# Optimization experiments

Measured on AMD Instinct MI355X. Metric: run time of the kernel, lower is better.

Reference implementation:

```python
import jax, jax.numpy as jnp
import numpy as np

LAMBDA_K_TAU = 0.1
RIDGE = 0.1


def _masked_cov(x, mask, counts):
    """Covariance of masked rows. x: [B,S,D], mask: [B,S] float, counts: [B] float.
    Equivalent to packing the masked rows (batch_2d_tensor) then _torch_cov."""
    xm = x * mask[..., None]
    mean = xm.sum(axis=1) / counts[:, None]                 # [B,D]
    xc = (xm - mean[:, None, :]) * mask[..., None]          # [B,S,D]
    cov = jnp.einsum('bsi,bsj->bij', xc, xc)
    return cov / (counts - 1.0)[:, None, None]


def _calc_label_cov_inv(task_cov, label_cov):
    d = task_cov.shape[-1]
    eye = jnp.eye(d, dtype=task_cov.dtype)
    return jnp.linalg.inv(LAMBDA_K_TAU * label_cov + (1.0 - LAMBDA_K_TAU) * task_cov + RIDGE * eye)


def setup_inputs() -> dict:
    key = jax.random.key(0)
    ks = jax.random.split(key, 6)
    B, S, Q, D = 256, 512, 256, 512
    support_set = jax.random.normal(ks[0], (B, S, D), dtype=jnp.float32)
    support_labels = jax.random.randint(ks[1], (B, S), 0, 2, dtype=jnp.int32)
    query_set = jax.random.normal(ks[2], (B, Q, D), dtype=jnp.float32)
    # lengths in [len//2, len] so both classes are present and counts > 1
    support_set_lengths = jax.random.randint(ks[3], (B,), S // 2, S + 1, dtype=jnp.int32)
    query_set_lengths = jax.random.randint(ks[4], (B,), Q // 2, Q + 1, dtype=jnp.int32)
    log_prediction_scaling = jnp.asarray(np.log(10.0), dtype=jnp.float32)
    return {
        'support_set': support_set,
        'support_labels': support_labels,
        'query_set': query_set,
        'support_set_lengths': support_set_lengths,
        'query_set_lengths': query_set_lengths,
        'log_prediction_scaling': log_prediction_scaling,
    }


def reference(support_set, support_labels, query_set, support_set_lengths,
              query_set_lengths, log_prediction_scaling):
    B, S, D = support_set.shape
    Q = query_set.shape[1]
    f32 = support_set.dtype

    sup_valid = (jnp.arange(S)[None, :] < support_set_lengths[:, None]).astype(f32)  # [B,S]
    mask_pos = (support_labels == 1).astype(f32) * sup_valid                          # [B,S]
    mask_neg = (support_labels == 0).astype(f32) * sup_valid

    pos_counts = mask_pos.sum(axis=1)   # [B]
    neg_counts = mask_neg.sum(axis=1)
    sup_counts = support_set_lengths.astype(f32)

    positive_mean = jnp.einsum('bsd,bs->bd', support_set, mask_pos) / pos_counts[:, None]
    negative_mean = jnp.einsum('bsd,bs->bd', support_set, mask_neg) / neg_counts[:, None]

    cov_mats = _masked_cov(support_set, sup_valid, sup_counts)   # task covariance
    pos_mats = _masked_cov(support_set, mask_pos, pos_counts)    # == cov of packed positives
    neg_mats = _masked_cov(support_set, mask_neg, neg_counts)

    pos_inv = _calc_label_cov_inv(cov_mats, pos_mats)  # [B,D,D]
    neg_inv = _calc_label_cov_inv(cov_mats, neg_mats)

    q_valid = (jnp.arange(Q)[None, :] < query_set_lengths[:, None]).astype(f32)  # [B,Q]

    pos_diff = positive_mean[:, None, :] - query_set  # [B,Q,D]
    neg_diff = negative_mean[:, None, :] - query_set
    pos_maha = jnp.einsum('bik,bkx,bix->bi', pos_diff, pos_inv, pos_diff) * q_valid
    neg_maha = jnp.einsum('bik,bkx,bix->bi', neg_diff, neg_inv, neg_diff) * q_valid

    logit_scale = jnp.exp(log_prediction_scaling)
    # scale is applied inside batch_calculate_mahalanobis_logits AND again in forward
    logits = jnp.stack([neg_maha, pos_maha], axis=-1) * (-1.0) * logit_scale
    return logits * logit_scale  # [B,Q,2]
```

## Files before the change

kernel.cpp:

```cpp
#include <hip/hip_runtime.h>
#include <hip/hip_bf16.h>

#define TPB 256
constexpr int B_ = 256, S_ = 512, D_ = 512, Q_ = 256, NM_ = 512;
constexpr int NB = 64, NT = 8;

typedef _Float16 f16x8 __attribute__((ext_vector_type(8)));
typedef float f32x4 __attribute__((ext_vector_type(4)));

__device__ __forceinline__ int pidx(int j, int a){ return j*(15-j)/2 + (a-j-1); }

__device__ __forceinline__ void decode_mt(int bid, int W, int& m, int& t){
  int x = bid & 7, r = bid >> 3;
  t = r % W; int u = r / W;
  m = (((u >> 1)*8 + x) << 1) | (u & 1);
}

__device__ __forceinline__ void stage_D(const float* __restrict__ src, size_t ld,
                                        float (*dst)[68], int t)
{
  int r = t >> 2, seg = (t & 3) * 16;
  const float4* s4 = (const float4*)(src + (size_t)r*ld + seg);
  #pragma unroll
  for (int i=0;i<4;i++) *((float4*)&dst[r][seg + i*4]) = s4[i];
}

__device__ __forceinline__ void mm_acc68(const float (*Aop)[68], const float (*Bop)[68],
                                         float acc[4][4], int tr, int tc)
{
  for (int kk=0;kk<64;kk++){
    float4 av = *((const float4*)&Aop[kk][tr*4]);
    float4 bv = *((const float4*)&Bop[kk][tc*4]);
    float a[4]={av.x,av.y,av.z,av.w}, b2[4]={bv.x,bv.y,bv.z,bv.w};
    #pragma unroll
    for (int u=0;u<4;u++)
      #pragma unroll
      for (int v=0;v<4;v++) acc[u][v] = fmaf(a[u], b2[v], acc[u][v]);
  }
}

__global__ __launch_bounds__(1024) void k_stats(const float* __restrict__ X,
                                                const int* __restrict__ labels,
                                                const int* __restrict__ slen,
                                                float* __restrict__ mu,
                                                float* __restrict__ cnt,
                                                unsigned int* __restrict__ wpbits)
{
  int b = blockIdx.x, t = threadIdx.x;
  int td = t & 255, sg = t >> 8;
  __shared__ int lab[S_];
  __shared__ float red[1024];
  __shared__ float part[4][256][4];
  int L = slen[b];
  if (t < S_) {
    int lb = labels[b*S_ + t];
    lab[t] = (t < L) ? lb : -1;
  }
  __syncthreads();
  if (t < 16) {
    unsigned int wword = 0;
    for (int i2 = 0; i2 < 32; i2++) if (lab[t*32 + i2] == 1) wword |= (1u << i2);
    wpbits[b*16 + t] = wword;
  }
  red[t] = (t < S_) ? ((lab[t]==1) ? 1.f : 0.f) : 0.f;
  __syncthreads();
  for (int o=512;o>0;o>>=1){ if(t<o) red[t]+=red[t+o]; __syncthreads(); }
  float cp = red[0]; __syncthreads();
  red[t] = (t < S_) ? ((lab[t]==0) ? 1.f : 0.f) : 0.f;
  __syncthreads();
  for (int o=512;o>0;o>>=1){ if(t<o) red[t]+=red[t+o]; __syncthreads(); }
  float cn = red[0];
  if (t==0){ cnt[b*2+0]=cn; cnt[b*2+1]=cp; }
  float sp0=0,sp1=0,sn0=0,sn1=0;
  const float* Xb = X + (size_t)b*S_*D_;
  for (int s=sg*128; s<sg*128+128; s++){
    int e = lab[s];
    if (e < 0) continue;
    float x0 = Xb[(size_t)s*D_ + td];
    float x1 = Xb[(size_t)s*D_ + td + 256];
    if (e==1){ sp0+=x0; sp1+=x1; } else { sn0+=x0; sn1+=x1; }
  }
  part[sg][td][0]=sn0; part[sg][td][1]=sn1; part[sg][td][2]=sp0; part[sg][td][3]=sp1;
  __syncthreads();
  if (sg == 0){
    float a0=0,a1=0,a2=0,a3=0;
    #pragma unroll
    for (int g=0;g<4;g++){ a0+=part[g][td][0]; a1+=part[g][td][1]; a2+=part[g][td][2]; a3+=part[g][td][3]; }
    float stv = (float)L;
    float* mb = mu + (size_t)b*3*D_;
    mb[0*D_ + td] = a0/cn;      mb[0*D_ + td+256] = a1/cn;
    mb[1*D_ + td] = a2/cp;      mb[1*D_ + td+256] = a3/cp;
    mb[2*D_ + td] = (a0+a2)/stv; mb[2*D_ + td+256] = (a1+a3)/stv;
  }
}

__global__ __launch_bounds__(TPB) void k_prep(const float* __restrict__ X,
                                              const int* __restrict__ slen,
                                              unsigned short* __restrict__ Xvh,
                                              unsigned short* __restrict__ Xvl)
{
  int b = blockIdx.y, z = blockIdx.x;
  int d0 = (z>>3)*64, s0 = (z&7)*64;
  int t = threadIdx.x;
  __shared__ float Tl[64][65];
  const float* src = X + ((size_t)b*S_ + s0)*D_ + d0;
  { int r = t>>2, seg = (t&3)*16;
    const float4* s4 = (const float4*)(src + (size_t)r*D_ + seg);
    #pragma unroll
    for (int i=0;i<4;i++){ float4 v = s4[i];
      Tl[seg+i*4+0][r]=v.x; Tl[seg+i*4+1][r]=v.y; Tl[seg+i*4+2][r]=v.z; Tl[seg+i*4+3][r]=v.w; } }
  __syncthreads();
  int L = slen[b];
  int dr = t>>2, sc = (t&3)*16;
  union U16 { unsigned short u[8]; uint4 v; };
  U16 H[2], Lo[2];
  #pragma unroll
  for (int g=0; g<2; g++)
    #pragma unroll
    for (int i=0;i<8;i++){
      int si = sc + g*8 + i;
      float x = (s0+si < L) ? Tl[dr][si] : 0.f;
      _Float16 hh = (_Float16)x;
      float lo = x - (float)hh;
      H[g].u[i]  = __builtin_bit_cast(unsigned short, hh);
      Lo[g].u[i] = __builtin_bit_cast(unsigned short, (_Float16)lo);
    }
  size_t o = ((size_t)b*D_ + d0+dr)*S_ + s0 + sc;
  *(uint4*)(Xvh+o)   = H[0].v;  *(uint4*)(Xvh+o+8) = H[1].v;
  *(uint4*)(Xvl+o)   = Lo[0].v; *(uint4*)(Xvl+o+8) = Lo[1].v;
}

__global__ __launch_bounds__(TPB,2) void k_gram(const unsigned short* __restrict__ Xvh,
                                                const unsigned short* __restrict__ Xvl,
                                                const unsigned int* __restrict__ wpbits,
                                                const float* __restrict__ mu,
                                                const float* __restrict__ cnt,
                                                const int* __restrict__ slen,
                                                float* __restrict__ A)
{
  __shared__ unsigned short sAvh[128][32], sAvl[128][32], sAph[128][32], sApl[128][32],
                            sBvh[128][32], sBvl[128][32];
  int id = blockIdx.x;
  int g = id>>3;
  int b = (g/10)*8 + (id&7);
  int z = g%10;
  int ti=0; while (z >= 4-ti){ z -= 4-ti; ti++; } int tj = ti + z;
  int i0 = ti*128, j0 = tj*128;
  int t = threadIdx.x, lane = t&63, w = t>>6;
  int wr = w>>1, wc = w&1, l15 = lane&15;

  f32x4 acc_t[4][4], acc_p[4][4];
  f32x4 z4 = {0.f,0.f,0.f,0.f};
  #pragma unroll
  for (int mf=0;mf<4;mf++)
    #pragma unroll
    for (int nf=0;nf<4;nf++){ acc_t[mf][nf]=z4; acc_p[mf][nf]=z4; }

  const size_t baseA = ((size_t)b*D_ + i0)*S_;
  const size_t baseB = ((size_t)b*D_ + j0)*S_;
  int phx = (lane>>4) ^ ((l15>>1)&3);

  for (int ks=0; ks<16; ks++){
    int s0 = ks*32;
    unsigned int wpw = wpbits[b*16 + ks];
    __syncthreads();
    #pragma unroll
    for (int h=0; h<2; h++){
      int ci = t + h*256;
      int row = ci>>2, cpos = ci&3;
      int ph = cpos ^ ((row>>1)&3);
      size_t ga = baseA + (size_t)row*S_ + s0 + cpos*8;
      size_t gb = baseB + (size_t)row*S_ + s0 + cpos*8;
      uint4 vh = *(const uint4*)(Xvh+ga);
      uint4 vl = *(const uint4*)(Xvl+ga);
      uint4 bh = *(const uint4*)(Xvh+gb);
      uint4 bl = *(const uint4*)(Xvl+gb);
      unsigned int m8 = (wpw >> (cpos*8)) & 0xFFu;
      uint4 mk;
      mk.x = ((m8&1u)?0xFFFFu:0u)  | ((m8&2u)?0xFFFF0000u:0u);
      mk.y = ((m8&4u)?0xFFFFu:0u)  | ((m8&8u)?0xFFFF0000u:0u);
      mk.z = ((m8&16u)?0xFFFFu:0u) | ((m8&32u)?0xFFFF0000u:0u);
      mk.w = ((m8&64u)?0xFFFFu:0u) | ((m8&128u)?0xFFFF0000u:0u);
      uint4 p4, q4;
      p4.x = vh.x&mk.x; p4.y = vh.y&mk.y; p4.z = vh.z&mk.z; p4.w = vh.w&mk.w;
      q4.x = vl.x&mk.x; q4.y = vl.y&mk.y; q4.z = vl.z&mk.z; q4.w = vl.w&mk.w;
      *(uint4*)&sAvh[row][ph*8] = vh;
      *(uint4*)&sAvl[row][ph*8] = vl;
      *(uint4*)&sAph[row][ph*8] = p4;
      *(uint4*)&sApl[row][ph*8] = q4;
      *(uint4*)&sBvh[row][ph*8] = bh;
      *(uint4*)&sBvl[row][ph*8] = bl;
    }
    __syncthreads();
    f16x8 Avh[4], Avl[4], Aph[4], Apl[4];
    #pragma unroll
    for (int mf=0;mf<4;mf++){
      int r = wr*64 + mf*16 + l15;
      Avh[mf] = __builtin_bit_cast(f16x8, *(const uint4*)&sAvh[r][phx*8]);
      Avl[mf] = __builtin_bit_cast(f16x8, *(const uint4*)&sAvl[r][phx*8]);
      Aph[mf] = __builtin_bit_cast(f16x8, *(const uint4*)&sAph[r][phx*8]);
      Apl[mf] = __builtin_bit_cast(f16x8, *(const uint4*)&sApl[r][phx*8]);
    }
    #pragma unroll
    for (int nf=0;nf<4;nf++){
      int r = wc*64 + nf*16 + l15;
      f16x8 Bh = __builtin_bit_cast(f16x8, *(const uint4*)&sBvh[r][phx*8]);
      f16x8 Bl = __builtin_bit_cast(f16x8, *(const uint4*)&sBvl[r][phx*8]);
      #pragma unroll
      for (int mf=0;mf<4;mf++){
        acc_t[mf][nf] = __builtin_amdgcn_mfma_f32_16x16x32_f16(Avh[mf], Bh, acc_t[mf][nf],0,0,0);
        acc_t[mf][nf] = __builtin_amdgcn_mfma_f32_16x16x32_f16(Avh[mf], Bl, acc_t[mf][nf],0,0,0);
        acc_t[mf][nf] = __builtin_amdgcn_mfma_f32_16x16x32_f16(Avl[mf], Bh, acc_t[mf][nf],0,0,0);
        acc_p[mf][nf] = __builtin_amdgcn_mfma_f32_16x16x32_f16(Aph[mf], Bh, acc_p[mf][nf],0,0,0);
        acc_p[mf][nf] = __builtin_amdgcn_mfma_f32_16x16x32_f16(Aph[mf], Bl, acc_p[mf][nf],0,0,0);
        acc_p[mf][nf] = __builtin_amdgcn_mfma_f32_16x16x32_f16(Apl[mf], Bh, acc_p[mf][nf],0,0,0);
      }
    }
  }
  float cn = cnt[b*2+0], cp = cnt[b*2+1];
  float stv = (float)slen[b];
  float kn = 0.1f/(cn-1.f), kp = 0.1f/(cp-1.f), kt = 0.9f/(stv-1.f);
  float rn = 0.1f*cn/(cn-1.f), rp = 0.1f*cp/(cp-1.f), rt = 0.9f*stv/(stv-1.f);
  const float* mb = mu + (size_t)b*3*D_;
  float* A0 = A + (size_t)(b*2+0)*D_*D_;
  float* A1 = A + (size_t)(b*2+1)*D_*D_;
  int rbase = i0 + wr*64 + (lane>>4)*4;
  int cbase = j0 + wc*64 + l15;
  #pragma unroll
  for (int mf=0;mf<4;mf++){
    #pragma unroll
    for (int i=0;i<4;i++){
      int r = rbase + mf*16 + i;
      float mnr = mb[r], mpr = mb[D_+r], mtr = mb[2*D_+r];
      #pragma unroll
      for (int nf=0;nf<4;nf++){
        int c = cbase + nf*16;
        float mnc = mb[c], mpc = mb[D_+c], mtc = mb[2*D_+c];
        float gp = acc_p[mf][nf][i];
        float gt = acc_t[mf][nf][i];
        float gn = gt - gp;
        float diag = (r==c)?0.1f:0.f;
        A0[(size_t)r*D_ + c] = kn*gn + kt*gt - rn*mnr*mnc - rt*mtr*mtc + diag;
        A1[(size_t)r*D_ + c] = kp*gp + kt*gt - rp*mpr*mpc - rt*mtr*mtc + diag;
      }
    }
  }
}

__global__ __launch_bounds__(TPB) void k_diag(float* __restrict__ A,
                                              float* __restrict__ invDT, int j)
{
  int m, t0; decode_mt(blockIdx.x, 1, m, t0); (void)t0;
  int t = threadIdx.x;
  __shared__ float Ld[64][65];
  __shared__ float Iv[64][65];
  float* Ab = A + (size_t)m*D_*D_ + (size_t)(j*NB)*D_ + j*NB;
  for (int l=t; l<4096; l+=TPB){ int r=l>>6, c=l&63; Ld[r][c] = Ab[(size_t)r*D_ + c]; Iv[r][c] = 0.f; }
  __syncthreads();
  for (int k=0;k<64;k++){
    if (t==0) Ld[k][k] = sqrtf(Ld[k][k]);
    __syncthreads();
    if (t>k && t<64) Ld[t][k] /= Ld[k][k];
    __syncthreads();
    for (int l=t; l<4096; l+=TPB){
      int r=l>>6, c=l&63;
      if (r>k && c>k) Ld[r][c] = fmaf(-Ld[r][k], Ld[c][k], Ld[r][c]);
    }
    __syncthreads();
  }
  if (t < 64){
    int c = t;
    Iv[c][c] = 1.f/Ld[c][c];
    for (int r=c+1;r<64;r++){
      float s = 0.f;
      for (int k2=c;k2<r;k2++) s += Ld[r][k2]*Iv[k2][c];
      Iv[r][c] = -s/Ld[r][r];
    }
  }
  __syncthreads();
  float* Ib = invDT + ((size_t)m*8 + j)*4096;
  for (int l=t; l<4096; l+=TPB){ Ib[l] = Iv[l&63][l>>6]; }
}

__global__ __launch_bounds__(TPB) void k_panel(float* __restrict__ A,
                                               const float* __restrict__ invDT,
                                               unsigned short* __restrict__ Ut,
                                               int j, int W)
{
  int m, ti; decode_mt(blockIdx.x, W, m, ti);
  int ib = j + 1 + ti;
  int t = threadIdx.x, tr = t&15, tc = t>>4;
  __shared__ float Ta[64][68], Tb[64][68];
  float* U = A + (size_t)m*D_*D_ + (size_t)(j*NB)*D_ + ib*NB;
  stage_D(invDT + ((size_t)m*8 + j)*4096, 64, Ta, t);
  stage_D(U, D_, Tb, t);
  __syncthreads();
  float acc[4][4] = {};
  mm_acc68(Ta, Tb, acc, tr, tc);
  #pragma unroll
  for (int u=0;u<4;u++){
    float4 o = make_float4(acc[u][0],acc[u][1],acc[u][2],acc[u][3]);
    *((float4*)(U + (size_t)(tr*4+u)*D_ + tc*4)) = o;
  }
  __syncthreads();
  unsigned short* shh = (unsigned short*)Ta;
  unsigned short* shl = (unsigned short*)Tb;
  #pragma unroll
  for (int u=0;u<4;u++)
    #pragma unroll
    for (int v=0;v<4;v++){
      float val = acc[u][v];
      _Float16 h = (_Float16)val;
      float lo = val - (float)h;
      shh[(tc*4+v)*72 + tr*4+u] = __builtin_bit_cast(unsigned short, h);
      shl[(tc*4+v)*72 + tr*4+u] = __builtin_bit_cast(unsigned short, (_Float16)lo);
    }
  __syncthreads();
  unsigned short* Ub = Ut + ((size_t)m*28 + pidx(j, ib)) * 8192;
  { int r = t>>2, cs = (t&3)*16;
    *(uint4*)(Ub + r*64 + cs)          = *(uint4*)&shh[r*72 + cs];
    *(uint4*)(Ub + r*64 + cs + 8)      = *(uint4*)&shh[r*72 + cs + 8];
    *(uint4*)(Ub + 4096 + r*64 + cs)   = *(uint4*)&shl[r*72 + cs];
    *(uint4*)(Ub + 4096 + r*64 + cs+8) = *(uint4*)&shl[r*72 + cs + 8];
  }
}

__device__ __forceinline__ void trail_stage(const unsigned short* __restrict__ Ua,
                                            const unsigned short* __restrict__ Ub,
                                            unsigned short (*Ah)[72], unsigned short (*Al)[72],
                                            unsigned short (*Bh)[72], unsigned short (*Bl)[72],
                                            int t)
{
  int r = t>>2, cs = (t&3)*16;
  *(uint4*)&Ah[r][cs]   = *(const uint4*)(Ua + r*64 + cs);
  *(uint4*)&Ah[r][cs+8] = *(const uint4*)(Ua + r*64 + cs + 8);
  *(uint4*)&Al[r][cs]   = *(const uint4*)(Ua + 4096 + r*64 + cs);
  *(uint4*)&Al[r][cs+8] = *(const uint4*)(Ua + 4096 + r*64 + cs + 8);
  *(uint4*)&Bh[r][cs]   = *(const uint4*)(Ub + r*64 + cs);
  *(uint4*)&Bh[r][cs+8] = *(const uint4*)(Ub + r*64 + cs + 8);
  *(uint4*)&Bl[r][cs]   = *(const uint4*)(Ub + 4096 + r*64 + cs);
  *(uint4*)&Bl[r][cs+8] = *(const uint4*)(Ub + 4096 + r*64 + cs + 8);
}

__device__ __forceinline__ void trail_mfma(const unsigned short (*Ah)[72], const unsigned short (*Al)[72],
                                           const unsigned short (*Bh)[72], const unsigned short (*Bl)[72],
                                           f32x4 acc[4], int w, int l15, int lk)
{
  #pragma unroll
  for (int s=0;s<2;s++){
    f16x8 Afh = __builtin_bit_cast(f16x8, *(const uint4*)&Ah[w*16 + l15][s*32 + lk*8]);
    f16x8 Afl = __builtin_bit_cast(f16x8, *(const uint4*)&Al[w*16 + l15][s*32 + lk*8]);
    #pragma unroll
    for (int ni=0;ni<4;ni++){
      f16x8 Bfh = __builtin_bit_cast(f16x8, *(const uint4*)&Bh[ni*16 + l15][s*32 + lk*8]);
      f16x8 Bfl = __builtin_bit_cast(f16x8, *(const uint4*)&Bl[ni*16 + l15][s*32 + lk*8]);
      acc[ni] = __builtin_amdgcn_mfma_f32_16x16x32_f16(Afh, Bfh, acc[ni],0,0,0);
      acc[ni] = __builtin_amdgcn_mfma_f32_16x16x32_f16(Afh, Bfl, acc[ni],0,0,0);
      acc[ni] = __builtin_amdgcn_mfma_f32_16x16x32_f16(Afl, Bfh, acc[ni],0,0,0);
    }
  }
}

__device__ __forceinline__ void trail_rmw(float* __restrict__ Cb, const f32x4 acc[4],
                                          int w, int l15, int lk)
{
  #pragma unroll
  for (int ni=0;ni<4;ni++)
    #pragma unroll
    for (int i=0;i<4;i++){
      int r = w*16 + lk*4 + i, cc = ni*16 + l15;
      float* pC = Cb + (size_t)r*D_ + cc;
      *pC -= acc[ni][i];
    }
}

__global__ __launch_bounds__(TPB) void k_trailrow(float* __restrict__ A,
                                                  const unsigned short* __restrict__ Ut,
                                                  int j, int row, int W)
{
  int m, z; decode_mt(blockIdx.x, W, m, z);
  int b2 = row + z;
  int t = threadIdx.x, lane = t&63, w = t>>6, l15 = lane&15, lk = lane>>4;
  __shared__ unsigned short Ah[64][72], Al[64][72], Bh[64][72], Bl[64][72];
  const unsigned short* Um = Ut + (size_t)m*28*8192;
  trail_stage(Um + (size_t)pidx(j,row)*8192, Um + (size_t)pidx(j,b2)*8192, Ah, Al, Bh, Bl, t);
  __syncthreads();
  f32x4 acc[4];
  #pragma unroll
  for (int ni=0;ni<4;ni++) acc[ni] = (f32x4){0.f,0.f,0.f,0.f};
  trail_mfma(Ah, Al, Bh, Bl, acc, w, l15, lk);
  float* Cb = A + (size_t)m*D_*D_ + (size_t)(row*NB)*D_ + b2*NB;
  trail_rmw(Cb, acc, w, l15, lk);
}

__global__ __launch_bounds__(TPB) void k_trail2(float* __restrict__ A,
                                                const unsigned short* __restrict__ Ut,
                                                int jb, int W)
{
  int m, z; decode_mt(blockIdx.x, W, m, z);
  int base = jb + 2;
  int Tn = NT - base;
  int p = 0, zz = z;
  while (zz >= Tn - p){ zz -= Tn - p; p++; }
  int a2 = base + p, b2 = a2 + zz;
  int t = threadIdx.x, lane = t&63, w = t>>6, l15 = lane&15, lk = lane>>4;
  __shared__ unsigned short Ah[64][72], Al[64][72], Bh[64][72], Bl[64][72];
  const unsigned short* Um = Ut + (size_t)m*28*8192;
  f32x4 acc[4];
  #pragma unroll
  for (int ni=0;ni<4;ni++) acc[ni] = (f32x4){0.f,0.f,0.f,0.f};
  #pragma unroll
  for (int c=0;c<2;c++){
    int j = jb + c;
    __syncthreads();
    trail_stage(Um + (size_t)pidx(j,a2)*8192, Um + (size_t)pidx(j,b2)*8192, Ah, Al, Bh, Bl, t);
    __syncthreads();
    trail_mfma(Ah, Al, Bh, Bl, acc, w, l15, lk);
  }
  float* Cb = A + (size_t)m*D_*D_ + (size_t)(a2*NB)*D_ + b2*NB;
  trail_rmw(Cb, acc, w, l15, lk);
}

__global__ __launch_bounds__(TPB) void k_solvefin(const float* __restrict__ Qs,
                                                  const float* __restrict__ mu,
                                                  const float* __restrict__ A,
                                                  const float* __restrict__ invDT,
                                                  float* __restrict__ Z,
                                                  const int* __restrict__ qlen,
                                                  const float* __restrict__ lps,
                                                  float* __restrict__ out)
{
  int m, t0; decode_mt(blockIdx.x, 4, m, t0);
  int q0 = t0*NB;
  int b = m>>1, cls = m&1;
  int t = threadIdx.x, tr = t&15, tc = t>>4;
  __shared__ float Ta[64][68], Tb[64][68];
  const float* Am = A + (size_t)m*D_*D_;
  float* Zm = Z + (size_t)m*D_*Q_;
  const float* muv = mu + ((size_t)b*3 + cls)*D_;
  float cs[4] = {0.f,0.f,0.f,0.f};
  for (int j=0;j<NT;j++){
    float acc[4][4];
    {
      float4 mv = *(const float4*)&muv[j*NB + tr*4];
      #pragma unroll
      for (int v=0;v<4;v++){
        float4 qv = *(const float4*)&Qs[((size_t)b*Q_ + q0 + tc*4 + v)*D_ + j*NB + tr*4];
        acc[0][v] = mv.x - qv.x;
        acc[1][v] = mv.y - qv.y;
        acc[2][v] = mv.z - qv.z;
        acc[3][v] = mv.w - qv.w;
      }
    }
    for (int k=0;k<j;k++){
      stage_D(Am + (size_t)(k*NB)*D_ + j*NB, D_, Ta, t);
      { int r = t >> 2, seg = (t & 3)*16;
        const float4* s4 = (const float4*)(Zm + (size_t)(k*NB + r)*Q_ + q0 + seg);
        #pragma unroll
        for (int i=0;i<4;i++) *((float4*)&Tb[r][seg + i*4]) = s4[i];
      }
      __syncthreads();
      for (int kk=0;kk<64;kk++){
        float4 av = *((const float4*)&Ta[kk][tr*4]);
        float4 bv = *((const float4*)&Tb[kk][tc*4]);
        float a[4]={av.x,av.y,av.z,av.w}, bb2[4]={bv.x,bv.y,bv.z,bv.w};
        #pragma unroll
        for (int u=0;u<4;u++)
          #pragma unroll
          for (int v=0;v<4;v++) acc[u][v] = fmaf(-a[u], bb2[v], acc[u][v]);
      }
      __syncthreads();
    }
    #pragma unroll
    for (int u=0;u<4;u++)
      #pragma unroll
      for (int v=0;v<4;v++) Tb[tr*4+u][tc*4+v] = acc[u][v];
    stage_D(invDT + ((size_t)m*8 + j)*4096, 64, Ta, t);
    __syncthreads();
    float o4[4][4] = {};
    for (int kk=0;kk<64;kk++){
      float4 av = *((const float4*)&Ta[kk][tr*4]);
      float4 bv = *((const float4*)&Tb[kk][tc*4]);
      float a[4]={av.x,av.y,av.z,av.w}, bb2[4]={bv.x,bv.y,bv.z,bv.w};
      #pragma unroll
      for (int u=0;u<4;u++)
        #pragma unroll
        for (int v=0;v<4;v++) o4[u][v] = fmaf(a[u], bb2[v], o4[u][v]);
    }
    if (j < NT-1){
      #pragma unroll
      for (int u=0;u<4;u++){
        float4 o = make_float4(o4[u][0], o4[u][1], o4[u][2], o4[u][3]);
        *((float4*)(Zm + (size_t)(j*NB + tr*4+u)*Q_ + q0 + tc*4)) = o;
      }
    }
    #pragma unroll
    for (int u=0;u<4;u++)
      #pragma unroll
      for (int v=0;v<4;v++) cs[v] = fmaf(o4[u][v], o4[u][v], cs[v]);
    __syncthreads();
  }
  float* red = &Ta[0][0];
  #pragma unroll
  for (int v=0;v<4;v++) red[(tc*4+v)*16 + tr] = cs[v];
  __syncthreads();
  if (t < 64){
    float s = 0.f;
    #pragma unroll
    for (int i=0;i<16;i++) s += red[t*16 + i];
    int q = q0 + t;
    float valid = (q < qlen[b]) ? 1.f : 0.f;
    float s2 = expf(2.f*lps[0]);
    out[((size_t)b*Q_ + q)*2 + cls] = -s2*s*valid;
  }
}

extern "C" void kernel_launch(void* const* d_in, const int* in_sizes, int n_in,
                              void* d_out, int out_size, void* d_ws, size_t ws_size,
                              hipStream_t stream) {
  (void)in_sizes; (void)n_in; (void)out_size;
  const float* X   = (const float*)d_in[0];
  const int*   lab = (const int*)d_in[1];
  const float* Qs  = (const float*)d_in[2];
  const int*   sl  = (const int*)d_in[3];
  const int*   ql  = (const int*)d_in[4];
  const float* lps = (const float*)d_in[5];
  float* out = (float*)d_out;

  float* A  = (float*)d_ws;
  float* Z  = A + (size_t)NM_*D_*D_;
  unsigned short* Xvh = (unsigned short*)Z;
  unsigned short* Xvl = Xvh + (size_t)B_*D_*S_;
  unsigned short* Ut  = (unsigned short*)Z;
  float* invDT = Z + (size_t)NM_*D_*Q_;
  float* mu   = invDT + (size_t)NM_*8*64*64;
  float* cnt  = mu + (size_t)B_*3*D_;
  unsigned int* wpbits = (unsigned int*)(cnt + B_*2);
  size_t need = (size_t)((char*)(wpbits + B_*16) - (char*)d_ws);
  if (ws_size < need) return;

  k_stats<<<dim3(B_), dim3(1024), 0, stream>>>(X, lab, sl, mu, cnt, wpbits);
  k_prep<<<dim3(64, B_), dim3(TPB), 0, stream>>>(X, sl, Xvh, Xvl);
  k_gram<<<dim3(2560), dim3(TPB), 0, stream>>>(Xvh, Xvl, wpbits, mu, cnt, sl, A);

  for (int j=0; j<NT; j+=2){
    k_diag<<<dim3(NM_), dim3(TPB), 0, stream>>>(A, invDT, j);
    int nb0 = NT-1-j;
    if (nb0 > 0){
      k_panel<<<dim3(NM_*nb0), dim3(TPB), 0, stream>>>(A, invDT, Ut, j, nb0);
      int wr = NT - (j+1);
      k_trailrow<<<dim3(NM_*wr), dim3(TPB), 0, stream>>>(A, Ut, j, j+1, wr);
      k_diag<<<dim3(NM_), dim3(TPB), 0, stream>>>(A, invDT, j+1);
      int nb1 = NT-1-(j+1);
      if (nb1 > 0){
        k_panel<<<dim3(NM_*nb1), dim3(TPB), 0, stream>>>(A, invDT, Ut, j+1, nb1);
        int Tn = NT - (j+2);
        int np = Tn*(Tn+1)/2;
        if (np > 0) k_trail2<<<dim3(NM_*np), dim3(TPB), 0, stream>>>(A, Ut, j, np);
      }
    }
  }

  k_solvefin<<<dim3(NM_*4), dim3(TPB), 0, stream>>>(Qs, mu, A, invDT, Z, ql, lps, out);
}
```

Before: 2.445 ms.

## Fuse diagonal Cholesky factor into trailing-update kernels and widen solve tiles

Removes the standalone diagonal-factor launches by having the trailing-update block that owns the next diagonal tile (z==0) apply its update in shared memory and factor/invert it in place, so that tile is never written back and re-read. The triangular inverse is parallelised across four lanes per column with shuffle reductions instead of one thread per column. The final solve kernel now handles 128 queries per block instead of 64, reusing each staged factor tile across twice as many columns. The trade-off is that the z==0 blocks become much longer than their siblings, the grid-stride structure creates tail imbalance, and the solve kernel uses more registers, which may lower occupancy.

New measurement: 2.681 ms. 1.1x slower.

```diff
diff --git a/kernel.cpp b/kernel.cpp
--- a/kernel.cpp
+++ b/kernel.cpp
@@ -247,39 +247,57 @@
   }
 }
 
-__global__ __launch_bounds__(TPB) void k_diag(float* __restrict__ A,
-                                              float* __restrict__ invDT, int j)
-{
-  int m, t0; decode_mt(blockIdx.x, 1, m, t0); (void)t0;
-  int t = threadIdx.x;
-  __shared__ float Ld[64][65];
-  __shared__ float Iv[64][65];
-  float* Ab = A + (size_t)m*D_*D_ + (size_t)(j*NB)*D_ + j*NB;
-  for (int l=t; l<4096; l+=TPB){ int r=l>>6, c=l&63; Ld[r][c] = Ab[(size_t)r*D_ + c]; Iv[r][c] = 0.f; }
-  __syncthreads();
+__device__ __forceinline__ void diag_finish(float* Ld, float* __restrict__ Ig, int t)
+{
   for (int k=0;k<64;k++){
-    if (t==0) Ld[k][k] = sqrtf(Ld[k][k]);
-    __syncthreads();
-    if (t>k && t<64) Ld[t][k] /= Ld[k][k];
+    if (t==0) Ld[k*68+k] = sqrtf(Ld[k*68+k]);
+    __syncthreads();
+    if (t>k && t<64) Ld[t*68+k] /= Ld[k*68+k];
     __syncthreads();
     for (int l=t; l<4096; l+=TPB){
       int r=l>>6, c=l&63;
-      if (r>k && c>k) Ld[r][c] = fmaf(-Ld[r][k], Ld[c][k], Ld[r][c]);
-    }
-    __syncthreads();
-  }
-  if (t < 64){
-    int c = t;
-    Iv[c][c] = 1.f/Ld[c][c];
-    for (int r=c+1;r<64;r++){
-      float s = 0.f;
-      for (int k2=c;k2<r;k2++) s += Ld[r][k2]*Iv[k2][c];
-      Iv[r][c] = -s/Ld[r][r];
-    }
-  }
-  __syncthreads();
-  float* Ib = invDT + ((size_t)m*8 + j)*4096;
-  for (int l=t; l<4096; l+=TPB){ Ib[l] = Iv[l&63][l>>6]; }
+      if (r>k && c>k) Ld[r*68+c] = fmaf(-Ld[r*68+k], Ld[c*68+k], Ld[r*68+c]);
+    }
+    __syncthreads();
+  }
+  int c = t>>2, s = t&3;
+  float myv[16];
+  #pragma unroll
+  for (int i=0;i<16;i++) myv[i] = 0.f;
+  if (s==0) myv[0] = 1.f/Ld[c*68+c];
+  for (int r=c+1;r<64;r++){
+    float partial = 0.f;
+    #pragma unroll
+    for (int idx=0; idx<16; idx++){
+      int k2 = c + s + 4*idx;
+      if (k2 < r) partial = fmaf(Ld[r*68+k2], myv[idx], partial);
+    }
+    partial += __shfl_xor(partial, 1, 64);
+    partial += __shfl_xor(partial, 2, 64);
+    float val = -partial / Ld[r*68+r];
+    int d = r - c;
+    #pragma unroll
+    for (int idx=0; idx<16; idx++)
+      if ((d & 3) == s && (d >> 2) == idx) myv[idx] = val;
+  }
+  #pragma unroll
+  for (int idx=0; idx<16; idx++){
+    int k2 = c + s + 4*idx;
+    if (k2 < 64) Ig[c*64 + k2] = myv[idx];
+  }
+}
+
+__global__ __launch_bounds__(TPB) void k_diag0(float* __restrict__ A, float* __restrict__ invDT)
+{
+  int m, du; decode_mt(blockIdx.x, 1, m, du); (void)du;
+  int t = threadIdx.x;
+  __shared__ float Ld[64*68];
+  const float* Cd = A + (size_t)m*D_*D_;
+  { int r = t>>2, seg = (t&3)*16;
+    #pragma unroll
+    for (int i=0;i<4;i++) *((float4*)&Ld[r*68 + seg + i*4]) = *((const float4*)(Cd + (size_t)r*D_ + seg + i*4)); }
+  __syncthreads();
+  diag_finish(Ld, invDT + (size_t)m*8*4096, t);
 }
 
 __global__ __launch_bounds__(TPB) void k_panel(float* __restrict__ A,
@@ -374,14 +392,37 @@
     }
 }
 
+__device__ __forceinline__ void fused_diag(float* __restrict__ A, float* __restrict__ invDT,
+                                           float* Ld, const f32x4 acc[4],
+                                           int m, int dblk, int t, int w, int l15, int lk)
+{
+  const float* Cd = A + (size_t)m*D_*D_ + (size_t)(dblk*NB)*D_ + dblk*NB;
+  { int r = t>>2, seg = (t&3)*16;
+    #pragma unroll
+    for (int i=0;i<4;i++) *((float4*)&Ld[r*68 + seg + i*4]) = *((const float4*)(Cd + (size_t)r*D_ + seg + i*4)); }
+  __syncthreads();
+  #pragma unroll
+  for (int ni=0;ni<4;ni++)
+    #pragma unroll
+    for (int i=0;i<4;i++)
+      Ld[(w*16 + lk*4 + i)*68 + ni*16 + l15] -= acc[ni][i];
+  __syncthreads();
+  diag_finish(Ld, invDT + ((size_t)m*8 + dblk)*4096, t);
+}
+
 __global__ __launch_bounds__(TPB) void k_trailrow(float* __restrict__ A,
                                                   const unsigned short* __restrict__ Ut,
+                                                  float* __restrict__ invDT,
                                                   int j, int row, int W)
 {
   int m, z; decode_mt(blockIdx.x, W, m, z);
   int b2 = row + z;
   int t = threadIdx.x, lane = t&63, w = t>>6, l15 = lane&15, lk = lane>>4;
-  __shared__ unsigned short Ah[64][72], Al[64][72], Bh[64][72], Bl[64][72];
+  __shared__ unsigned short sbuf[4*64*72];
+  unsigned short (*Ah)[72] = (unsigned short(*)[72])sbuf;
+  unsigned short (*Al)[72] = (unsigned short(*)[72])(sbuf + 64*72);
+  unsigned short (*Bh)[72] = (unsigned short(*)[72])(sbuf + 2*64*72);
+  unsigned short (*Bl)[72] = (unsigned short(*)[72])(sbuf + 3*64*72);
   const unsigned short* Um = Ut + (size_t)m*28*8192;
   trail_stage(Um + (size_t)pidx(j,row)*8192, Um + (size_t)pidx(j,b2)*8192, Ah, Al, Bh, Bl, t);
   __syncthreads();
@@ -389,12 +430,18 @@
   #pragma unroll
   for (int ni=0;ni<4;ni++) acc[ni] = (f32x4){0.f,0.f,0.f,0.f};
   trail_mfma(Ah, Al, Bh, Bl, acc, w, l15, lk);
-  float* Cb = A + (size_t)m*D_*D_ + (size_t)(row*NB)*D_ + b2*NB;
-  trail_rmw(Cb, acc, w, l15, lk);
+  if (z == 0){
+    __syncthreads();
+    fused_diag(A, invDT, (float*)sbuf, acc, m, row, t, w, l15, lk);
+  } else {
+    float* Cb = A + (size_t)m*D_*D_ + (size_t)(row*NB)*D_ + b2*NB;
+    trail_rmw(Cb, acc, w, l15, lk);
+  }
 }
 
 __global__ __launch_bounds__(TPB) void k_trail2(float* __restrict__ A,
                                                 const unsigned short* __restrict__ Ut,
+                                                float* __restrict__ invDT,
                                                 int jb, int W)
 {
   int m, z; decode_mt(blockIdx.x, W, m, z);
@@ -404,7 +451,11 @@
   while (zz >= Tn - p){ zz -= Tn - p; p++; }
   int a2 = base + p, b2 = a2 + zz;
   int t = threadIdx.x, lane = t&63, w = t>>6, l15 = lane&15, lk = lane>>4;
-  __shared__ unsigned short Ah[64][72], Al[64][72], Bh[64][72], Bl[64][72];
+  __shared__ unsigned short sbuf[4*64*72];
+  unsigned short (*Ah)[72] = (unsigned short(*)[72])sbuf;
+  unsigned short (*Al)[72] = (unsigned short(*)[72])(sbuf + 64*72);
+  unsigned short (*Bh)[72] = (unsigned short(*)[72])(sbuf + 2*64*72);
+  unsigned short (*Bl)[72] = (unsigned short(*)[72])(sbuf + 3*64*72);
   const unsigned short* Um = Ut + (size_t)m*28*8192;
   f32x4 acc[4];
   #pragma unroll
@@ -417,8 +468,13 @@
     __syncthreads();
     trail_mfma(Ah, Al, Bh, Bl, acc, w, l15, lk);
   }
-  float* Cb = A + (size_t)m*D_*D_ + (size_t)(a2*NB)*D_ + b2*NB;
-  trail_rmw(Cb, acc, w, l15, lk);
+  if (z == 0){
+    __syncthreads();
+    fused_diag(A, invDT, (float*)sbuf, acc, m, base, t, w, l15, lk);
+  } else {
+    float* Cb = A + (size_t)m*D_*D_ + (size_t)(a2*NB)*D_ + b2*NB;
+    trail_rmw(Cb, acc, w, l15, lk);
+  }
 }
 
 __global__ __launch_bounds__(TPB) void k_solvefin(const float* __restrict__ Qs,
@@ -430,81 +486,105 @@
                                                   const float* __restrict__ lps,
                                                   float* __restrict__ out)
 {
-  int m, t0; decode_mt(blockIdx.x, 4, m, t0);
-  int q0 = t0*NB;
+  int m, t0; decode_mt(blockIdx.x, 2, m, t0);
+  int q0 = t0*128;
   int b = m>>1, cls = m&1;
   int t = threadIdx.x, tr = t&15, tc = t>>4;
-  __shared__ float Ta[64][68], Tb[64][68];
+  __shared__ float Ta[64][68];
+  __shared__ float Tb[64][136];
   const float* Am = A + (size_t)m*D_*D_;
   float* Zm = Z + (size_t)m*D_*Q_;
   const float* muv = mu + ((size_t)b*3 + cls)*D_;
-  float cs[4] = {0.f,0.f,0.f,0.f};
+  float cs[2][4] = {};
   for (int j=0;j<NT;j++){
-    float acc[4][4];
+    float acc[2][4][4];
     {
       float4 mv = *(const float4*)&muv[j*NB + tr*4];
       #pragma unroll
-      for (int v=0;v<4;v++){
-        float4 qv = *(const float4*)&Qs[((size_t)b*Q_ + q0 + tc*4 + v)*D_ + j*NB + tr*4];
-        acc[0][v] = mv.x - qv.x;
-        acc[1][v] = mv.y - qv.y;
-        acc[2][v] = mv.z - qv.z;
-        acc[3][v] = mv.w - qv.w;
-      }
+      for (int h=0;h<2;h++)
+        #pragma unroll
+        for (int v=0;v<4;v++){
+          float4 qv = *(const float4*)&Qs[((size_t)b*Q_ + q0 + h*64 + tc*4 + v)*D_ + j*NB + tr*4];
+          acc[h][0][v] = mv.x - qv.x;
+          acc[h][1][v] = mv.y - qv.y;
+          acc[h][2][v] = mv.z - qv.z;
+          acc[h][3][v] = mv.w - qv.w;
+        }
     }
     for (int k=0;k<j;k++){
       stage_D(Am + (size_t)(k*NB)*D_ + j*NB, D_, Ta, t);
       { int r = t >> 2, seg = (t & 3)*16;
-        const float4* s4 = (const float4*)(Zm + (size_t)(k*NB + r)*Q_ + q0 + seg);
         #pragma unroll
-        for (int i=0;i<4;i++) *((float4*)&Tb[r][seg + i*4]) = s4[i];
+        for (int h=0;h<2;h++){
+          const float4* s4 = (const float4*)(Zm + (size_t)(k*NB + r)*Q_ + q0 + h*64 + seg);
+          #pragma unroll
+          for (int i=0;i<4;i++) *((float4*)&Tb[r][h*68 + seg + i*4]) = s4[i];
+        }
       }
       __syncthreads();
       for (int kk=0;kk<64;kk++){
         float4 av = *((const float4*)&Ta[kk][tr*4]);
-        float4 bv = *((const float4*)&Tb[kk][tc*4]);
-        float a[4]={av.x,av.y,av.z,av.w}, bb2[4]={bv.x,bv.y,bv.z,bv.w};
+        float4 bv0 = *((const float4*)&Tb[kk][tc*4]);
+        float4 bv1 = *((const float4*)&Tb[kk][68 + tc*4]);
+        float a[4]={av.x,av.y,av.z,av.w};
+        float b0[4]={bv0.x,bv0.y,bv0.z,bv0.w}, b1[4]={bv1.x,bv1.y,bv1.z,bv1.w};
         #pragma unroll
         for (int u=0;u<4;u++)
           #pragma unroll
-          for (int v=0;v<4;v++) acc[u][v] = fmaf(-a[u], bb2[v], acc[u][v]);
+          for (int v=0;v<4;v++){
+            acc[0][u][v] = fmaf(-a[u], b0[v], acc[0][u][v]);
+            acc[1][u][v] = fmaf(-a[u], b1[v], acc[1][u][v]);
+          }
       }
       __syncthreads();
     }
     #pragma unroll
-    for (int u=0;u<4;u++)
-      #pragma unroll
-      for (int v=0;v<4;v++) Tb[tr*4+u][tc*4+v] = acc[u][v];
+    for (int h=0;h<2;h++)
+      #pragma unroll
+      for (int u=0;u<4;u++)
+        #pragma unroll
+        for (int v=0;v<4;v++) Tb[tr*4+u][h*68 + tc*4+v] = acc[h][u][v];
     stage_D(invDT + ((size_t)m*8 + j)*4096, 64, Ta, t);
     __syncthreads();
-    float o4[4][4] = {};
+    float o4[2][4][4] = {};
     for (int kk=0;kk<64;kk++){
       float4 av = *((const float4*)&Ta[kk][tr*4]);
-      float4 bv = *((const float4*)&Tb[kk][tc*4]);
-      float a[4]={av.x,av.y,av.z,av.w}, bb2[4]={bv.x,bv.y,bv.z,bv.w};
+      float4 bv0 = *((const float4*)&Tb[kk][tc*4]);
+      float4 bv1 = *((const float4*)&Tb[kk][68 + tc*4]);
+      float a[4]={av.x,av.y,av.z,av.w};
+      float b0[4]={bv0.x,bv0.y,bv0.z,bv0.w}, b1[4]={bv1.x,bv1.y,bv1.z,bv1.w};
       #pragma unroll
       for (int u=0;u<4;u++)
         #pragma unroll
-        for (int v=0;v<4;v++) o4[u][v] = fmaf(a[u], bb2[v], o4[u][v]);
+        for (int v=0;v<4;v++){
+          o4[0][u][v] = fmaf(a[u], b0[v], o4[0][u][v]);
+          o4[1][u][v] = fmaf(a[u], b1[v], o4[1][u][v]);
+        }
     }
     if (j < NT-1){
       #pragma unroll
-      for (int u=0;u<4;u++){
-        float4 o = make_float4(o4[u][0], o4[u][1], o4[u][2], o4[u][3]);
-        *((float4*)(Zm + (size_t)(j*NB + tr*4+u)*Q_ + q0 + tc*4)) = o;
-      }
-    }
-    #pragma unroll
-    for (int u=0;u<4;u++)
-      #pragma unroll
-      for (int v=0;v<4;v++) cs[v] = fmaf(o4[u][v], o4[u][v], cs[v]);
-    __syncthreads();
-  }
-  float* red = &Ta[0][0];
-  #pragma unroll
-  for (int v=0;v<4;v++) red[(tc*4+v)*16 + tr] = cs[v];
-  __syncthreads();
-  if (t < 64){
+      for (int h=0;h<2;h++)
+        #pragma unroll
+        for (int u=0;u<4;u++){
+          float4 o = make_float4(o4[h][u][0], o4[h][u][1], o4[h][u][2], o4[h][u][3]);
+          *((float4*)(Zm + (size_t)(j*NB + tr*4+u)*Q_ + q0 + h*64 + tc*4)) = o;
+        }
+    }
+    #pragma unroll
+    for (int h=0;h<2;h++)
+      #pragma unroll
+      for (int u=0;u<4;u++)
+        #pragma unroll
+        for (int v=0;v<4;v++) cs[h][v] = fmaf(o4[h][u][v], o4[h][u][v], cs[h][v]);
+    __syncthreads();
+  }
+  float* red = &Tb[0][0];
+  #pragma unroll
+  for (int h=0;h<2;h++)
+    #pragma unroll
+    for (int v=0;v<4;v++) red[(h*64 + tc*4+v)*16 + tr] = cs[h][v];
+  __syncthreads();
+  if (t < 128){
     float s = 0.f;
     #pragma unroll
     for (int i=0;i<16;i++) s += red[t*16 + i];
@@ -543,23 +623,20 @@
   k_prep<<<dim3(64, B_), dim3(TPB), 0, stream>>>(X, sl, Xvh, Xvl);
   k_gram<<<dim3(2560), dim3(TPB), 0, stream>>>(Xvh, Xvl, wpbits, mu, cnt, sl, A);
 
+  k_diag0<<<dim3(NM_), dim3(TPB), 0, stream>>>(A, invDT);
   for (int j=0; j<NT; j+=2){
-    k_diag<<<dim3(NM_), dim3(TPB), 0, stream>>>(A, invDT, j);
     int nb0 = NT-1-j;
-    if (nb0 > 0){
-      k_panel<<<dim3(NM_*nb0), dim3(TPB), 0, stream>>>(A, invDT, Ut, j, nb0);
-      int wr = NT - (j+1);
-      k_trailrow<<<dim3(NM_*wr), dim3(TPB), 0, stream>>>(A, Ut, j, j+1, wr);
-      k_diag<<<dim3(NM_), dim3(TPB), 0, stream>>>(A, invDT, j+1);
-      int nb1 = NT-1-(j+1);
-      if (nb1 > 0){
-        k_panel<<<dim3(NM_*nb1), dim3(TPB), 0, stream>>>(A, invDT, Ut, j+1, nb1);
-        int Tn = NT - (j+2);
-        int np = Tn*(Tn+1)/2;
-        if (np > 0) k_trail2<<<dim3(NM_*np), dim3(TPB), 0, stream>>>(A, Ut, j, np);
-      }
-    }
-  }
-
-  k_solvefin<<<dim3(NM_*4), dim3(TPB), 0, stream>>>(Qs, mu, A, invDT, Z, ql, lps, out);
-}
+    k_panel<<<dim3(NM_*nb0), dim3(TPB), 0, stream>>>(A, invDT, Ut, j, nb0);
+    int wr = NT-1-j;
+    k_trailrow<<<dim3(NM_*wr), dim3(TPB), 0, stream>>>(A, Ut, invDT, j, j+1, wr);
+    int nb1 = NT-1-(j+1);
+    if (nb1 > 0){
+      k_panel<<<dim3(NM_*nb1), dim3(TPB), 0, stream>>>(A, invDT, Ut, j+1, nb1);
+      int Tn = NT - (j+2);
+      int np = Tn*(Tn+1)/2;
+      if (np > 0) k_trail2<<<dim3(NM_*np), dim3(TPB), 0, stream>>>(A, Ut, invDT, j, np);
+    }
+  }
+
+  k_solvefin<<<dim3(NM_*2), dim3(TPB), 0, stream>>>(Qs, mu, A, invDT, Z, ql, lps, out);
+}
```

## Fuse stats kernel into prep pass and swizzle Tb shared tile

Applied to the files above, without the earlier changes.

The separate stats kernel, which read X once to compute class means and counts, is folded into the prep kernel. The prep kernel now loops over all S tiles per 64-column d block and accumulates the per-class sums while it converts X into hi/lo fp16 pieces. This removes one full read of the support set and one launch, but the grid shrinks from 64×B to 8×B blocks, each doing serial work. Separately, the Tb tile write and read in a later kernel use an XOR swizzle to reduce LDS bank conflicts.

Result: faster. 2.392 ms (median of 2 runs) (-2.2%).

```diff
diff --git a/kernel.cpp b/kernel.cpp
--- a/kernel.cpp
+++ b/kernel.cpp
@@ -39,95 +39,92 @@
   }
 }
 
-__global__ __launch_bounds__(1024) void k_stats(const float* __restrict__ X,
-                                                const int* __restrict__ labels,
-                                                const int* __restrict__ slen,
-                                                float* __restrict__ mu,
-                                                float* __restrict__ cnt,
-                                                unsigned int* __restrict__ wpbits)
-{
-  int b = blockIdx.x, t = threadIdx.x;
-  int td = t & 255, sg = t >> 8;
+__global__ __launch_bounds__(TPB) void k_prep(const float* __restrict__ X,
+                                              const int* __restrict__ labels,
+                                              const int* __restrict__ slen,
+                                              unsigned short* __restrict__ Xvh,
+                                              unsigned short* __restrict__ Xvl,
+                                              float* __restrict__ mu,
+                                              float* __restrict__ cnt,
+                                              unsigned int* __restrict__ wpbits)
+{
+  int b = blockIdx.y, dz = blockIdx.x;
+  int d0 = dz*64;
+  int t = threadIdx.x;
+  __shared__ float Tl[64][65];
   __shared__ int lab[S_];
-  __shared__ float red[1024];
-  __shared__ float part[4][256][4];
+  __shared__ float red[TPB];
   int L = slen[b];
-  if (t < S_) {
-    int lb = labels[b*S_ + t];
-    lab[t] = (t < L) ? lb : -1;
-  }
-  __syncthreads();
-  if (t < 16) {
+  for (int s = t; s < S_; s += TPB){
+    int lb = labels[b*S_ + s];
+    lab[s] = (s < L) ? lb : -1;
+  }
+  __syncthreads();
+  if (dz == 0 && t < 16){
     unsigned int wword = 0;
-    for (int i2 = 0; i2 < 32; i2++) if (lab[t*32 + i2] == 1) wword |= (1u << i2);
-    wpbits[b*16 + t] = wword;
-  }
-  red[t] = (t < S_) ? ((lab[t]==1) ? 1.f : 0.f) : 0.f;
-  __syncthreads();
-  for (int o=512;o>0;o>>=1){ if(t<o) red[t]+=red[t+o]; __syncthreads(); }
+    for (int i2=0;i2<32;i2++) if (lab[t*32+i2]==1) wword |= (1u<<i2);
+    wpbits[b*16+t] = wword;
+  }
+  int cpi=0, cni=0;
+  for (int s=t; s<S_; s+=TPB){ cpi += (lab[s]==1); cni += (lab[s]==0); }
+  red[t] = (float)cpi; __syncthreads();
+  for (int o=TPB/2;o>0;o>>=1){ if(t<o) red[t]+=red[t+o]; __syncthreads(); }
   float cp = red[0]; __syncthreads();
-  red[t] = (t < S_) ? ((lab[t]==0) ? 1.f : 0.f) : 0.f;
-  __syncthreads();
-  for (int o=512;o>0;o>>=1){ if(t<o) red[t]+=red[t+o]; __syncthreads(); }
+  red[t] = (float)cni; __syncthreads();
+  for (int o=TPB/2;o>0;o>>=1){ if(t<o) red[t]+=red[t+o]; __syncthreads(); }
   float cn = red[0];
-  if (t==0){ cnt[b*2+0]=cn; cnt[b*2+1]=cp; }
-  float sp0=0,sp1=0,sn0=0,sn1=0;
-  const float* Xb = X + (size_t)b*S_*D_;
-  for (int s=sg*128; s<sg*128+128; s++){
-    int e = lab[s];
-    if (e < 0) continue;
-    float x0 = Xb[(size_t)s*D_ + td];
-    float x1 = Xb[(size_t)s*D_ + td + 256];
-    if (e==1){ sp0+=x0; sp1+=x1; } else { sn0+=x0; sn1+=x1; }
-  }
-  part[sg][td][0]=sn0; part[sg][td][1]=sn1; part[sg][td][2]=sp0; part[sg][td][3]=sp1;
-  __syncthreads();
-  if (sg == 0){
-    float a0=0,a1=0,a2=0,a3=0;
-    #pragma unroll
-    for (int g=0;g<4;g++){ a0+=part[g][td][0]; a1+=part[g][td][1]; a2+=part[g][td][2]; a3+=part[g][td][3]; }
+  if (dz==0 && t==0){ cnt[b*2+0]=cn; cnt[b*2+1]=cp; }
+  __syncthreads();
+
+  int dr = t>>2, sc = (t&3)*16;
+  float accp = 0.f, accn = 0.f;
+  for (int sz=0; sz<8; sz++){
+    int s0 = sz*64;
+    const float* src = X + ((size_t)b*S_ + s0)*D_ + d0;
+    { int r = t>>2, seg = (t&3)*16;
+      const float4* s4 = (const float4*)(src + (size_t)r*D_ + seg);
+      #pragma unroll
+      for (int i=0;i<4;i++){ float4 v = s4[i];
+        Tl[seg+i*4+0][r]=v.x; Tl[seg+i*4+1][r]=v.y; Tl[seg+i*4+2][r]=v.z; Tl[seg+i*4+3][r]=v.w; } }
+    __syncthreads();
+    union U16 { unsigned short u[8]; uint4 v; };
+    U16 H[2], Lo[2];
+    #pragma unroll
+    for (int g=0; g<2; g++)
+      #pragma unroll
+      for (int i=0;i<8;i++){
+        int si = sc + g*8 + i;
+        float x = (s0+si < L) ? Tl[dr][si] : 0.f;
+        _Float16 hh = (_Float16)x;
+        float lo = x - (float)hh;
+        H[g].u[i]  = __builtin_bit_cast(unsigned short, hh);
+        Lo[g].u[i] = __builtin_bit_cast(unsigned short, (_Float16)lo);
+      }
+    size_t o = ((size_t)b*D_ + d0+dr)*S_ + s0 + sc;
+    *(uint4*)(Xvh+o)   = H[0].v;  *(uint4*)(Xvh+o+8) = H[1].v;
+    *(uint4*)(Xvl+o)   = Lo[0].v; *(uint4*)(Xvl+o+8) = Lo[1].v;
+    #pragma unroll
+    for (int i=0;i<16;i++){
+      int si = sc + i;
+      int e = lab[s0+si];
+      float x = Tl[dr][si];
+      accp += (e==1) ? x : 0.f;
+      accn += (e==0) ? x : 0.f;
+    }
+    __syncthreads();
+  }
+  accp += __shfl_xor(accp, 1, 64);
+  accp += __shfl_xor(accp, 2, 64);
+  accn += __shfl_xor(accn, 1, 64);
+  accn += __shfl_xor(accn, 2, 64);
+  if ((t&3)==0){
+    int d = d0 + dr;
     float stv = (float)L;
     float* mb = mu + (size_t)b*3*D_;
-    mb[0*D_ + td] = a0/cn;      mb[0*D_ + td+256] = a1/cn;
-    mb[1*D_ + td] = a2/cp;      mb[1*D_ + td+256] = a3/cp;
-    mb[2*D_ + td] = (a0+a2)/stv; mb[2*D_ + td+256] = (a1+a3)/stv;
-  }
-}
-
-__global__ __launch_bounds__(TPB) void k_prep(const float* __restrict__ X,
-                                              const int* __restrict__ slen,
-                                              unsigned short* __restrict__ Xvh,
-                                              unsigned short* __restrict__ Xvl)
-{
-  int b = blockIdx.y, z = blockIdx.x;
-  int d0 = (z>>3)*64, s0 = (z&7)*64;
-  int t = threadIdx.x;
-  __shared__ float Tl[64][65];
-  const float* src = X + ((size_t)b*S_ + s0)*D_ + d0;
-  { int r = t>>2, seg = (t&3)*16;
-    const float4* s4 = (const float4*)(src + (size_t)r*D_ + seg);
-    #pragma unroll
-    for (int i=0;i<4;i++){ float4 v = s4[i];
-      Tl[seg+i*4+0][r]=v.x; Tl[seg+i*4+1][r]=v.y; Tl[seg+i*4+2][r]=v.z; Tl[seg+i*4+3][r]=v.w; } }
-  __syncthreads();
-  int L = slen[b];
-  int dr = t>>2, sc = (t&3)*16;
-  union U16 { unsigned short u[8]; uint4 v; };
-  U16 H[2], Lo[2];
-  #pragma unroll
-  for (int g=0; g<2; g++)
-    #pragma unroll
-    for (int i=0;i<8;i++){
-      int si = sc + g*8 + i;
-      float x = (s0+si < L) ? Tl[dr][si] : 0.f;
-      _Float16 hh = (_Float16)x;
-      float lo = x - (float)hh;
-      H[g].u[i]  = __builtin_bit_cast(unsigned short, hh);
-      Lo[g].u[i] = __builtin_bit_cast(unsigned short, (_Float16)lo);
-    }
-  size_t o = ((size_t)b*D_ + d0+dr)*S_ + s0 + sc;
-  *(uint4*)(Xvh+o)   = H[0].v;  *(uint4*)(Xvh+o+8) = H[1].v;
-  *(uint4*)(Xvl+o)   = Lo[0].v; *(uint4*)(Xvl+o+8) = Lo[1].v;
+    mb[0*D_ + d] = accn/cn;
+    mb[1*D_ + d] = accp/cp;
+    mb[2*D_ + d] = (accn+accp)/stv;
+  }
 }
 
 __global__ __launch_bounds__(TPB,2) void k_gram(const unsigned short* __restrict__ Xvh,
@@ -472,15 +469,16 @@
       __syncthreads();
     }
     #pragma unroll
-    for (int u=0;u<4;u++)
-      #pragma unroll
-      for (int v=0;v<4;v++) Tb[tr*4+u][tc*4+v] = acc[u][v];
+    for (int u=0;u<4;u++){
+      int cb = (tc*4) ^ ((tr&7)<<2);
+      *((float4*)&Tb[tr*4+u][cb]) = make_float4(acc[u][0],acc[u][1],acc[u][2],acc[u][3]);
+    }
     stage_D(invDT + ((size_t)m*8 + j)*4096, 64, Ta, t);
     __syncthreads();
     float o4[4][4] = {};
     for (int kk=0;kk<64;kk++){
       float4 av = *((const float4*)&Ta[kk][tr*4]);
-      float4 bv = *((const float4*)&Tb[kk][tc*4]);
+      float4 bv = *((const float4*)&Tb[kk][(tc*4) ^ (((kk>>2)&7)<<2)]);
       float a[4]={av.x,av.y,av.z,av.w}, bb2[4]={bv.x,bv.y,bv.z,bv.w};
       #pragma unroll
       for (int u=0;u<4;u++)
@@ -539,8 +537,7 @@
   size_t need = (size_t)((char*)(wpbits + B_*16) - (char*)d_ws);
   if (ws_size < need) return;
 
-  k_stats<<<dim3(B_), dim3(1024), 0, stream>>>(X, lab, sl, mu, cnt, wpbits);
-  k_prep<<<dim3(64, B_), dim3(TPB), 0, stream>>>(X, sl, Xvh, Xvl);
+  k_prep<<<dim3(8, B_), dim3(TPB), 0, stream>>>(X, lab, sl, Xvh, Xvl, mu, cnt, wpbits);
   k_gram<<<dim3(2560), dim3(TPB), 0, stream>>>(Xvh, Xvl, wpbits, mu, cnt, sl, A);
 
   for (int j=0; j<NT; j+=2){
```
